# Performance work log

Hardware: AMD Instinct MI355X
Metric: run time of the kernel (lower is better)

The kernel has to match this reference:

```python
import jax, jax.numpy as jnp
import numpy as np

V, C, L, H, FF, T_MAX = 50257, 768, 12, 12, 3072, 1024
D = C // H  # head_dim = 64
B, T = 4, 1024


def setup_inputs() -> dict:
    key = jax.random.key(0)
    ks = jax.random.split(key, 20)
    s = 0.02
    inp = {
        'input_ids': jax.random.randint(ks[0], (B, T), 0, V),
        'tok_emb': jax.random.normal(ks[1], (V, C), jnp.float32) * s,
        'pos_emb': jax.random.normal(ks[2], (T_MAX, C), jnp.float32) * s,
        # per-layer stacked params; linear weights stored [in, out] (torch W.T)
        'qkv_w': jax.random.normal(ks[3], (L, C, 3 * C), jnp.float32) * s,
        'qkv_b': jnp.zeros((L, 3 * C), jnp.float32),
        'proj_w': jax.random.normal(ks[4], (L, C, C), jnp.float32) * (s / np.sqrt(2 * L)),
        'proj_b': jnp.zeros((L, C), jnp.float32),
        'ln1_w': jnp.ones((L, C), jnp.float32),
        'ln1_b': jnp.zeros((L, C), jnp.float32),
        'ln2_w': jnp.ones((L, C), jnp.float32),
        'ln2_b': jnp.zeros((L, C), jnp.float32),
        'fc1_w': jax.random.normal(ks[5], (L, C, FF), jnp.float32) * s,
        'fc1_b': jnp.zeros((L, FF), jnp.float32),
        'fc2_w': jax.random.normal(ks[6], (L, FF, C), jnp.float32) * s,
        'fc2_b': jnp.zeros((L, C), jnp.float32),
        'lnf_w': jnp.ones((C,), jnp.float32),
        'lnf_b': jnp.zeros((C,), jnp.float32),
    }
    return inp


def _ln(x, w, b, eps=1e-5):
    mu = jnp.mean(x, axis=-1, keepdims=True)
    var = jnp.var(x, axis=-1, keepdims=True)
    return (x - mu) * jax.lax.rsqrt(var + eps) * w + b


def _gpt_forward(input_ids, tok_emb, pos_emb, qkv_w, qkv_b, proj_w, proj_b,
                 ln1_w, ln1_b, ln2_w, ln2_b, fc1_w, fc1_b, fc2_w, fc2_b,
                 lnf_w, lnf_b):
    Bc, Tc = input_ids.shape
    x = tok_emb[input_ids] + pos_emb[:Tc][None, :, :]  # [B,T,C]
    causal = jnp.tril(jnp.ones((Tc, Tc), bool))  # [T,T]
    scale = 1.0 / np.sqrt(D)

    def block(x, p):
        (qw, qb, pw, pb, l1w, l1b, l2w, l2b, f1w, f1b, f2w, f2b) = p
        h = _ln(x, l1w, l1b)
        qkv = h @ qw + qb  # [B,T,3C]
        q, k, v = jnp.split(qkv, 3, axis=-1)
        q = q.reshape(Bc, Tc, H, D)
        k = k.reshape(Bc, Tc, H, D)
        v = v.reshape(Bc, Tc, H, D)
        att = jnp.einsum('bqhd,bkhd->bhqk', q, k) * scale
        att = jnp.where(causal[None, None], att, -jnp.inf)
        att = jax.nn.softmax(att, axis=-1)
        o = jnp.einsum('bhqk,bkhd->bqhd', att, v).reshape(Bc, Tc, C)
        x = x + o @ pw + pb
        h2 = _ln(x, l2w, l2b)
        m = jax.nn.gelu(h2 @ f1w + f1b, approximate=False) @ f2w + f2b
        return x + m, None

    params = (qkv_w, qkv_b, proj_w, proj_b, ln1_w, ln1_b, ln2_w, ln2_b,
              fc1_w, fc1_b, fc2_w, fc2_b)
    x, _ = jax.lax.scan(block, x, params)
    x = _ln(x, lnf_w, lnf_b)
    logits = x @ tok_emb.T  # tied lm_head, no bias
    return logits


def reference(input_ids, tok_emb, pos_emb, qkv_w, qkv_b, proj_w, proj_b,
              ln1_w, ln1_b, ln2_w, ln2_b, fc1_w, fc1_b, fc2_w, fc2_b,
              lnf_w, lnf_b):
    return _gpt_forward(input_ids, tok_emb, pos_emb, qkv_w, qkv_b, proj_w,
                        proj_b, ln1_w, ln1_b, ln2_w, ln2_b, fc1_w, fc1_b,
                        fc2_w, fc2_b, lnf_w, lnf_b)
```

## Files before the change

### kernel.cpp

```cpp
#include <hip/hip_runtime.h>
#include <hip/hip_bf16.h>


typedef __bf16 bh_t;
typedef __bf16 bfx4 __attribute__((ext_vector_type(4)));
typedef __bf16 bfx8 __attribute__((ext_vector_type(8)));
typedef float  fx4  __attribute__((ext_vector_type(4)));

#define CDIM 768
#define TSEQ 1024
#define NHEAD 12
#define HDIM 64
#define NLAYER 12
#define MROWS 4096
#define VOCAB 50257
#define VPAD  50432

__device__ __forceinline__ void gload_lds16(const void* g, void* l) {
  __builtin_amdgcn_global_load_lds(
      (const __attribute__((address_space(1))) void*)g,
      (__attribute__((address_space(3))) void*)l, 16, 0, 0);
}

__device__ __forceinline__ fx4 mfma16(bfx8 a, bfx8 b, fx4 c) {
  return __builtin_amdgcn_mfma_f32_16x16x32_bf16(a, b, c, 0, 0, 0);
}

__global__ __launch_bounds__(512, 1) void gemm256(
    const bh_t* __restrict__ A, const bh_t* __restrict__ B,
    const float* __restrict__ bias, void* __restrict__ outp,
    int M, int N, int K, int lda, int flags)
{
  __shared__ bh_t LA0[2][128][64], LB0[2][128][64];
  __shared__ bh_t LA1[2][128][64], LB1[2][128][64];
  const int tid = threadIdx.x;
  const int wid = tid >> 6, lane = tid & 63;
  const int g = lane >> 4, r16 = lane & 15;
  const int wr = wid >> 2, wc = wid & 3;
  const int m0 = blockIdx.x * 256, n0 = blockIdx.y * 256;
  const int sw0 = ((g     ) ^ (r16 & 7)) * 8;
  const int sw1 = ((g + 4) ^ (r16 & 7)) * 8;

  const bh_t* Ab = A + (size_t)blockIdx.z * K + (size_t)m0 * lda;
  const bh_t* Bb = B + (size_t)blockIdx.z * K + (size_t)n0 * lda;
  const bh_t* Ab1 = Ab + (size_t)128 * lda;
  const bh_t* Bb1 = Bb + (size_t)128 * lda;
  const int nt = K >> 6;

  fx4 acc[8][4] = {};

  auto stageHalf = [&](bh_t* dst, const bh_t* src, int t) {
    const int k0 = t << 6;
    #pragma unroll
    for (int j = 0; j < 2; ++j) {
      const int idx = j * 512 + tid;
      const int row = idx >> 3;
      const int slot = (idx & 7) ^ (row & 7);
      gload_lds16(src + (size_t)row * lda + k0 + slot * 8, dst + (size_t)idx * 8);
    }
  };

#define LM_TILE(CA, CB, NA, NB, T)                                            \
  {                                                                           \
    const bh_t* ca = &CA[wr][0][0];                                           \
    const bh_t* cb = &CB[wc >> 1][0][0] + (size_t)((wc & 1) * 64) * 64;       \
    bfx8 a0[4], b0[4], b1[4];                                                 \
                                       \
    _Pragma("unroll")                                                         \
    for (int ni = 0; ni < 4; ++ni)                                            \
      b0[ni] = *(const bfx8*)(cb + (size_t)(ni * 16 + r16) * 64 + sw0);       \
    _Pragma("unroll")                                                         \
    for (int mi = 0; mi < 4; ++mi)                                            \
      a0[mi] = *(const bfx8*)(ca + (size_t)(mi * 16 + r16) * 64 + sw0);       \
    __builtin_amdgcn_s_setprio(1);                                            \
    _Pragma("unroll")                                                         \
    for (int mi = 0; mi < 4; ++mi)                                            \
      _Pragma("unroll")                                                       \
      for (int ni = 0; ni < 4; ++ni)                                          \
        acc[mi][ni] = mfma16(a0[mi], b0[ni], acc[mi][ni]);                    \
    __builtin_amdgcn_s_setprio(0);                                            \
                                        \
    if ((T) + 1 < nt) stageHalf(&NA[1][0][0], Ab1, (T) + 1);                  \
    _Pragma("unroll")                                                         \
    for (int mi = 0; mi < 4; ++mi)                                            \
      a0[mi] = *(const bfx8*)(ca + (size_t)(64 + mi * 16 + r16) * 64 + sw0);  \
    __builtin_amdgcn_s_setprio(1);                                            \
    _Pragma("unroll")                                                         \
    for (int mi = 0; mi < 4; ++mi)                                            \
      _Pragma("unroll")                                                       \
      for (int ni = 0; ni < 4; ++ni)                                          \
        acc[4 + mi][ni] = mfma16(a0[mi], b0[ni], acc[4 + mi][ni]);            \
    __builtin_amdgcn_s_setprio(0);                                            \
                                \
    if ((T) + 1 < nt) stageHalf(&NB[0][0][0], Bb, (T) + 1);                   \
    _Pragma("unroll")                                                         \
    for (int ni = 0; ni < 4; ++ni)                                            \
      b1[ni] = *(const bfx8*)(cb + (size_t)(ni * 16 + r16) * 64 + sw1);       \
    _Pragma("unroll")                                                         \
    for (int mi = 0; mi < 4; ++mi)                                            \
      a0[mi] = *(const bfx8*)(ca + (size_t)(mi * 16 + r16) * 64 + sw1);       \
    __builtin_amdgcn_s_setprio(1);                                            \
    _Pragma("unroll")                                                         \
    for (int mi = 0; mi < 4; ++mi)                                            \
      _Pragma("unroll")                                                       \
      for (int ni = 0; ni < 4; ++ni)                                          \
        acc[mi][ni] = mfma16(a0[mi], b1[ni], acc[mi][ni]);                    \
    __builtin_amdgcn_s_setprio(0);                                            \
                                        \
    if ((T) + 1 < nt) stageHalf(&NB[1][0][0], Bb1, (T) + 1);                  \
    _Pragma("unroll")                                                         \
    for (int mi = 0; mi < 4; ++mi)                                            \
      a0[mi] = *(const bfx8*)(ca + (size_t)(64 + mi * 16 + r16) * 64 + sw1);  \
    __builtin_amdgcn_s_setprio(1);                                            \
    _Pragma("unroll")                                                         \
    for (int mi = 0; mi < 4; ++mi)                                            \
      _Pragma("unroll")                                                       \
      for (int ni = 0; ni < 4; ++ni)                                          \
        acc[4 + mi][ni] = mfma16(a0[mi], b1[ni], acc[4 + mi][ni]);            \
    __builtin_amdgcn_s_setprio(0);                                            \
                                                                \
    asm volatile("s_waitcnt lgkmcnt(0)" ::: "memory");                        \
    __builtin_amdgcn_s_barrier();                                             \
    if ((T) + 2 < nt) {                                                       \
      stageHalf(&CA[0][0][0], Ab, (T) + 2);                                   \
      asm volatile("s_waitcnt vmcnt(2)" ::: "memory");                        \
    } else if ((T) + 1 < nt) {                                                \
      asm volatile("s_waitcnt vmcnt(0)" ::: "memory");                        \
    }                                                                         \
    __builtin_amdgcn_s_barrier();                                             \
    asm volatile("" ::: "memory");                                            \
  }

  stageHalf(&LA0[0][0][0], Ab, 0);
  stageHalf(&LA0[1][0][0], Ab1, 0);
  stageHalf(&LB0[0][0][0], Bb, 0);
  stageHalf(&LB0[1][0][0], Bb1, 0);
  stageHalf(&LA1[0][0][0], Ab, 1);
  asm volatile("s_waitcnt vmcnt(2)" ::: "memory");
  __builtin_amdgcn_s_barrier();
  asm volatile("" ::: "memory");

  for (int t = 0; t < nt; t += 2) {
    LM_TILE(LA0, LB0, LA1, LB1, t);
    LM_TILE(LA1, LB1, LA0, LB0, t + 1);
  }
#undef LM_TILE

  const bool hasBias = flags & 1, doGelu = flags & 4, outBf = flags & 8;
  float* outF = (float*)outp + (size_t)blockIdx.z * ((size_t)M * N);
  bh_t*  outB = (bh_t*)outp;
  #pragma unroll
  for (int mi = 0; mi < 8; ++mi) {
    const int rowb = m0 + wr * 128 + mi * 16 + 4 * g;
    #pragma unroll
    for (int ni = 0; ni < 4; ++ni) {
      const int col = n0 + wc * 64 + ni * 16 + r16;
      if (col >= N) continue;
      const float bv = hasBias ? bias[col] : 0.0f;
      #pragma unroll
      for (int rr = 0; rr < 4; ++rr) {
        const size_t idx = (size_t)(rowb + rr) * N + col;
        float v = acc[mi][ni][rr] + bv;
        if (doGelu) v = 0.5f * v * (1.0f + erff(v * 0.70710678118654752f));
        if (outBf) outB[idx] = (bh_t)v; else outF[idx] = v;
      }
    }
  }
}

__global__ __launch_bounds__(256, 3) void gemm_bt(
    const bh_t* __restrict__ A, const bh_t* __restrict__ B,
    const float* __restrict__ bias, const float* __restrict__ resid,
    void* __restrict__ outp, int M, int N, int K, int lda, int flags)
{
  __shared__ bh_t As0[4][128][8], Bs0[4][128][8];
  __shared__ bh_t As1[4][128][8], Bs1[4][128][8];
  __shared__ bh_t As2[4][128][8], Bs2[4][128][8];
  const int tid  = threadIdx.x;
  const int wave = tid >> 6, lane = tid & 63;
  const int g = lane >> 4, r16 = lane & 15;
  const int m0 = blockIdx.x * 128, n0 = blockIdx.y * 128;
  const int wm = (wave >> 1) * 64, wn = (wave & 1) * 64;

  const bh_t* Ab = A;
  const bh_t* Bb = B;
  if (gridDim.z > 1) {
    Ab += (size_t)blockIdx.z * K;
    Bb += (size_t)blockIdx.z * K;
  }
  Ab += (size_t)m0 * lda;
  Bb += (size_t)n0 * lda;

  const int row0 = tid & 127, kb0 = tid >> 7;
  const int kb1 = kb0 + 2;

  fx4 acc[4][4] = {};
  const int nk = K >> 5;

  auto stageTo = [&](bh_t* AsF, bh_t* BsF, int t) {
    const int k0 = t << 5;
    gload_lds16(Ab + (size_t)row0 * lda + k0 + kb0 * 8, AsF + (size_t)(wave * 64) * 8);
    gload_lds16(Ab + (size_t)row0 * lda + k0 + kb1 * 8, AsF + (size_t)(256 + wave * 64) * 8);
    gload_lds16(Bb + (size_t)row0 * lda + k0 + kb0 * 8, BsF + (size_t)(wave * 64) * 8);
    gload_lds16(Bb + (size_t)row0 * lda + k0 + kb1 * 8, BsF + (size_t)(256 + wave * 64) * 8);
  };

#define GPT_PHASE(CURA, CURB, NXA, NXB, T)                                   \
  {                                                                          \
    if ((T) + 1 < nk) { asm volatile("s_waitcnt vmcnt(4)" ::: "memory"); }   \
    else              { asm volatile("s_waitcnt vmcnt(0)" ::: "memory"); }   \
    __builtin_amdgcn_s_barrier();                                            \
    asm volatile("" ::: "memory");                                           \
    if ((T) + 2 < nk) stageTo(&NXA[0][0][0], &NXB[0][0][0], (T) + 2);        \
    bfx8 af[4], bfr[4];                                                      \
    _Pragma("unroll")                                                        \
    for (int mi = 0; mi < 4; ++mi)                                           \
      af[mi] = *(const bfx8*)&CURA[g][wm + mi * 16 + r16][0];                \
    _Pragma("unroll")                                                        \
    for (int ni = 0; ni < 4; ++ni)                                           \
      bfr[ni] = *(const bfx8*)&CURB[g][wn + ni * 16 + r16][0];               \
    _Pragma("unroll")                                                        \
    for (int mi = 0; mi < 4; ++mi)                                           \
      _Pragma("unroll")                                                      \
      for (int ni = 0; ni < 4; ++ni)                                         \
        acc[mi][ni] = mfma16(af[mi], bfr[ni], acc[mi][ni]);                  \
  }

  stageTo(&As0[0][0][0], &Bs0[0][0][0], 0);
  stageTo(&As1[0][0][0], &Bs1[0][0][0], 1);
  for (int t = 0; t < nk; t += 3) {
    GPT_PHASE(As0, Bs0, As2, Bs2, t);
    GPT_PHASE(As1, Bs1, As0, Bs0, t + 1);
    GPT_PHASE(As2, Bs2, As1, Bs1, t + 2);
  }
#undef GPT_PHASE

  const bool hasBias = flags & 1, hasRes = flags & 2;
  const bool doGelu  = flags & 4, outBf  = flags & 8;
  float* outF = (float*)outp + (size_t)blockIdx.z * ((size_t)M * N);
  bh_t*  outB = (bh_t*)outp;
  #pragma unroll
  for (int mi = 0; mi < 4; ++mi) {
    #pragma unroll
    for (int ni = 0; ni < 4; ++ni) {
      const int col = n0 + wn + ni * 16 + r16;
      if (col >= N) continue;
      const int rowb = m0 + wm + mi * 16 + 4 * g;
      const float bv = hasBias ? bias[col] : 0.0f;
      #pragma unroll
      for (int rr = 0; rr < 4; ++rr) {
        const size_t idx = (size_t)(rowb + rr) * N + col;
        float v = acc[mi][ni][rr] + bv;
        if (doGelu) v = 0.5f * v * (1.0f + erff(v * 0.70710678118654752f));
        if (hasRes) v += resid[idx];
        if (outBf) outB[idx] = (bh_t)v; else outF[idx] = v;
      }
    }
  }
}

__global__ __launch_bounds__(256) void skred_ln(
    const float* __restrict__ part, const float* __restrict__ bias,
    float* __restrict__ x, const float* __restrict__ w,
    const float* __restrict__ bb, bh_t* __restrict__ out, int S)
{
  const int wave = threadIdx.x >> 6, lane = threadIdx.x & 63;
  const int row = blockIdx.x * 4 + wave;
  const size_t base = (size_t)row * CDIM;
  const int off = lane * 4;
  const size_t stride = (size_t)MROWS * CDIM;

  float4 v0 = *(const float4*)(x + base + off);
  float4 v1 = *(const float4*)(x + base + 256 + off);
  float4 v2 = *(const float4*)(x + base + 512 + off);
  for (int s = 0; s < S; ++s) {
    const float* pr = part + s * stride + base;
    const float4 p0 = *(const float4*)(pr + off);
    const float4 p1 = *(const float4*)(pr + 256 + off);
    const float4 p2 = *(const float4*)(pr + 512 + off);
    v0.x += p0.x; v0.y += p0.y; v0.z += p0.z; v0.w += p0.w;
    v1.x += p1.x; v1.y += p1.y; v1.z += p1.z; v1.w += p1.w;
    v2.x += p2.x; v2.y += p2.y; v2.z += p2.z; v2.w += p2.w;
  }
  const float4 q0 = *(const float4*)(bias + off);
  const float4 q1 = *(const float4*)(bias + 256 + off);
  const float4 q2 = *(const float4*)(bias + 512 + off);
  v0.x += q0.x; v0.y += q0.y; v0.z += q0.z; v0.w += q0.w;
  v1.x += q1.x; v1.y += q1.y; v1.z += q1.z; v1.w += q1.w;
  v2.x += q2.x; v2.y += q2.y; v2.z += q2.z; v2.w += q2.w;
  *(float4*)(x + base + off) = v0;
  *(float4*)(x + base + 256 + off) = v1;
  *(float4*)(x + base + 512 + off) = v2;

  float s1 = v0.x + v0.y + v0.z + v0.w + v1.x + v1.y + v1.z + v1.w
           + v2.x + v2.y + v2.z + v2.w;
  float ss = v0.x*v0.x + v0.y*v0.y + v0.z*v0.z + v0.w*v0.w
           + v1.x*v1.x + v1.y*v1.y + v1.z*v1.z + v1.w*v1.w
           + v2.x*v2.x + v2.y*v2.y + v2.z*v2.z + v2.w*v2.w;
  #pragma unroll
  for (int d = 1; d < 64; d <<= 1) { s1 += __shfl_xor(s1, d); ss += __shfl_xor(ss, d); }
  const float mean = s1 * (1.0f / 768.0f);
  const float inv = rsqrtf(ss * (1.0f / 768.0f) - mean * mean + 1e-5f);
  bh_t* orow = out + base;

  const float4 w0 = *(const float4*)(w + off),       b0 = *(const float4*)(bb + off);
  const float4 w1 = *(const float4*)(w + 256 + off), b1 = *(const float4*)(bb + 256 + off);
  const float4 w2 = *(const float4*)(w + 512 + off), b2 = *(const float4*)(bb + 512 + off);
  bfx4 o;
  o[0] = (bh_t)((v0.x - mean) * inv * w0.x + b0.x);
  o[1] = (bh_t)((v0.y - mean) * inv * w0.y + b0.y);
  o[2] = (bh_t)((v0.z - mean) * inv * w0.z + b0.z);
  o[3] = (bh_t)((v0.w - mean) * inv * w0.w + b0.w);
  *(bfx4*)(orow + off) = o;
  o[0] = (bh_t)((v1.x - mean) * inv * w1.x + b1.x);
  o[1] = (bh_t)((v1.y - mean) * inv * w1.y + b1.y);
  o[2] = (bh_t)((v1.z - mean) * inv * w1.z + b1.z);
  o[3] = (bh_t)((v1.w - mean) * inv * w1.w + b1.w);
  *(bfx4*)(orow + 256 + off) = o;
  o[0] = (bh_t)((v2.x - mean) * inv * w2.x + b2.x);
  o[1] = (bh_t)((v2.y - mean) * inv * w2.y + b2.y);
  o[2] = (bh_t)((v2.z - mean) * inv * w2.z + b2.z);
  o[3] = (bh_t)((v2.w - mean) * inv * w2.w + b2.w);
  *(bfx4*)(orow + 512 + off) = o;
}

__global__ __launch_bounds__(256) void attn_fwd(
    const bh_t* __restrict__ qkv, const bh_t* __restrict__ vT,
    bh_t* __restrict__ outb)
{
  __shared__ bh_t P[4][16][56];
  const int wave = threadIdx.x >> 6, lane = threadIdx.x & 63;
  const int g = lane >> 4, r16 = lane & 15;
  const int gw = blockIdx.x * 4 + wave;
  const int qblk = gw & 63;
  const int bh = gw >> 6;
  const int h = bh % NHEAD, b = bh / NHEAD;
  const int qbase = qblk * 16;
  const int qidx = qbase + r16;

  const bh_t* qp = qkv + (size_t)(b * TSEQ + qbase + r16) * (3 * CDIM) + h * HDIM + 8 * g;
  const bfx8 qf0 = *(const bfx8*)qp;
  const bfx8 qf1 = *(const bfx8*)(qp + 32);

  fx4 o[4] = {};
  float m = -INFINITY, l = 0.0f;
  const int ntiles = qblk / 2 + 1;

  for (int t = 0; t < ntiles; ++t) {
    const int kv0 = t * 32;
    const bh_t* kp = qkv + (size_t)(b * TSEQ + kv0 + r16) * (3 * CDIM) + CDIM + h * HDIM + 8 * g;
    const bfx8 ka0 = *(const bfx8*)kp;
    const bfx8 ka1 = *(const bfx8*)(kp + 32);
    const bfx8 kb0 = *(const bfx8*)(kp + 16 * (3 * CDIM));
    const bfx8 kb1 = *(const bfx8*)(kp + 16 * (3 * CDIM) + 32);
    fx4 s0 = {}, s1 = {};
    s0 = mfma16(ka0, qf0, s0); s0 = mfma16(ka1, qf1, s0);
    s1 = mfma16(kb0, qf0, s1); s1 = mfma16(kb1, qf1, s1);

    float mx = -INFINITY;
    float sv0[4], sv1[4];
    #pragma unroll
    for (int rr = 0; rr < 4; ++rr) {
      const int kva = kv0 + 4 * g + rr;
      const int kvb = kva + 16;
      sv0[rr] = (kva <= qidx) ? s0[rr] * 0.125f : -INFINITY;
      sv1[rr] = (kvb <= qidx) ? s1[rr] * 0.125f : -INFINITY;
      mx = fmaxf(mx, fmaxf(sv0[rr], sv1[rr]));
    }
    mx = fmaxf(mx, __shfl_xor(mx, 16));
    mx = fmaxf(mx, __shfl_xor(mx, 32));
    const float mnew = fmaxf(m, mx);
    const float corr = __expf(m - mnew);

    float ps = 0.0f;
    float pv0[4], pv1[4];
    #pragma unroll
    for (int rr = 0; rr < 4; ++rr) {
      pv0[rr] = __expf(sv0[rr] - mnew);
      pv1[rr] = __expf(sv1[rr] - mnew);
      ps += pv0[rr] + pv1[rr];
    }
    ps += __shfl_xor(ps, 16);
    ps += __shfl_xor(ps, 32);
    l = l * corr + ps;
    m = mnew;

    #pragma unroll
    for (int rr = 0; rr < 4; ++rr) {
      const float cr = __shfl(corr, 4 * g + rr);
      o[0][rr] *= cr; o[1][rr] *= cr; o[2][rr] *= cr; o[3][rr] *= cr;
    }

    bfx4 w0, w1;
    #pragma unroll
    for (int rr = 0; rr < 4; ++rr) { w0[rr] = (bh_t)pv0[rr]; w1[rr] = (bh_t)pv1[rr]; }
    *(bfx4*)&P[wave][r16][4 * g]      = w0;
    *(bfx4*)&P[wave][r16][16 + 4 * g] = w1;
    __builtin_amdgcn_wave_barrier();
    const bfx8 pf = *(const bfx8*)&P[wave][r16][8 * g];

    #pragma unroll
    for (int fi = 0; fi < 4; ++fi) {
      const bh_t* vp = vT + (size_t)(bh * HDIM + fi * 16 + r16) * TSEQ + kv0 + 8 * g;
      const bfx8 vf = *(const bfx8*)vp;
      o[fi] = mfma16(pf, vf, o[fi]);
    }
  }

  #pragma unroll
  for (int rr = 0; rr < 4; ++rr) {
    const float lr = __shfl(l, 4 * g + rr);
    const float inv = 1.0f / lr;
    const int trow = b * TSEQ + qbase + 4 * g + rr;
    #pragma unroll
    for (int fi = 0; fi < 4; ++fi)
      outb[(size_t)trow * CDIM + h * HDIM + fi * 16 + r16] = (bh_t)(o[fi][rr] * inv);
  }
}

__global__ __launch_bounds__(256) void ln_fwd(
    const float* __restrict__ x, const float* __restrict__ w,
    const float* __restrict__ bb, bh_t* __restrict__ out)
{
  const int wave = threadIdx.x >> 6, lane = threadIdx.x & 63;
  const int row = blockIdx.x * 4 + wave;
  const float* xr = x + (size_t)row * CDIM;
  const int off = lane * 4;
  const float4 v0 = *(const float4*)(xr + off);
  const float4 v1 = *(const float4*)(xr + 256 + off);
  const float4 v2 = *(const float4*)(xr + 512 + off);
  float s  = v0.x + v0.y + v0.z + v0.w + v1.x + v1.y + v1.z + v1.w
           + v2.x + v2.y + v2.z + v2.w;
  float ss = v0.x*v0.x + v0.y*v0.y + v0.z*v0.z + v0.w*v0.w
           + v1.x*v1.x + v1.y*v1.y + v1.z*v1.z + v1.w*v1.w
           + v2.x*v2.x + v2.y*v2.y + v2.z*v2.z + v2.w*v2.w;
  #pragma unroll
  for (int d = 1; d < 64; d <<= 1) { s += __shfl_xor(s, d); ss += __shfl_xor(ss, d); }
  const float mean = s * (1.0f / 768.0f);
  const float inv = rsqrtf(ss * (1.0f / 768.0f) - mean * mean + 1e-5f);
  bh_t* orow = out + (size_t)row * CDIM;

  const float4 w0 = *(const float4*)(w + off),  b0 = *(const float4*)(bb + off);
  const float4 w1 = *(const float4*)(w + 256 + off), b1 = *(const float4*)(bb + 256 + off);
  const float4 w2 = *(const float4*)(w + 512 + off), b2 = *(const float4*)(bb + 512 + off);
  bfx4 o;
  o[0] = (bh_t)((v0.x - mean) * inv * w0.x + b0.x);
  o[1] = (bh_t)((v0.y - mean) * inv * w0.y + b0.y);
  o[2] = (bh_t)((v0.z - mean) * inv * w0.z + b0.z);
  o[3] = (bh_t)((v0.w - mean) * inv * w0.w + b0.w);
  *(bfx4*)(orow + off) = o;
  o[0] = (bh_t)((v1.x - mean) * inv * w1.x + b1.x);
  o[1] = (bh_t)((v1.y - mean) * inv * w1.y + b1.y);
  o[2] = (bh_t)((v1.z - mean) * inv * w1.z + b1.z);
  o[3] = (bh_t)((v1.w - mean) * inv * w1.w + b1.w);
  *(bfx4*)(orow + 256 + off) = o;
  o[0] = (bh_t)((v2.x - mean) * inv * w2.x + b2.x);
  o[1] = (bh_t)((v2.y - mean) * inv * w2.y + b2.y);
  o[2] = (bh_t)((v2.z - mean) * inv * w2.z + b2.z);
  o[3] = (bh_t)((v2.w - mean) * inv * w2.w + b2.w);
  *(bfx4*)(orow + 512 + off) = o;
}

__global__ void embed_k(const int* __restrict__ ids, const float* __restrict__ tok,
                        const float* __restrict__ pos, float* __restrict__ x)
{
  const int bt = blockIdx.x;
  const int t = bt & (TSEQ - 1);
  const int id = ids[bt];
  const float* tr = tok + (size_t)id * CDIM;
  const float* pr = pos + (size_t)t * CDIM;
  float* xr = x + (size_t)bt * CDIM;
  for (int j = threadIdx.x; j < CDIM; j += 256) xr[j] = tr[j] + pr[j];
}

__global__ void tconv(const float* __restrict__ in, bh_t* __restrict__ out, int R, int Cn)
{
  __shared__ float tile[32][33];
  const size_t msz = (size_t)R * Cn;
  in  += msz * blockIdx.z;
  out += msz * blockIdx.z;
  const int tx = threadIdx.x & 31, ty = threadIdx.x >> 5;
  const int c0 = blockIdx.x * 32, r0 = blockIdx.y * 32;
  #pragma unroll
  for (int i = 0; i < 32; i += 8)
    tile[ty + i][tx] = in[(size_t)(r0 + ty + i) * Cn + c0 + tx];
  __syncthreads();
  #pragma unroll
  for (int i = 0; i < 32; i += 8)
    out[(size_t)(c0 + ty + i) * R + r0 + tx] = (bh_t)tile[tx][ty + i];
}

__global__ void embconv(const float* __restrict__ in, bh_t* __restrict__ out)
{
  const size_t i4 = ((size_t)blockIdx.x * 256 + threadIdx.x) * 4;
  if (i4 >= (size_t)VPAD * CDIM) return;
  const size_t vlim = (size_t)VOCAB * CDIM;
  float4 f = make_float4(0.f, 0.f, 0.f, 0.f);
  if (i4 < vlim) f = *(const float4*)(in + i4);
  bfx4 o;
  o[0] = (bh_t)f.x; o[1] = (bh_t)f.y; o[2] = (bh_t)f.z; o[3] = (bh_t)f.w;
  *(bfx4*)(out + i4) = o;
}

__global__ void vtrans(const bh_t* __restrict__ qkv, bh_t* __restrict__ vT)
{
  __shared__ bh_t tile[32][34];
  const int bh = blockIdx.z;
  const int b = bh / NHEAD, h = bh % NHEAD;
  const int d0 = blockIdx.x * 32, t0 = blockIdx.y * 32;
  const int tx = threadIdx.x & 31, ty = threadIdx.x >> 5;
  #pragma unroll
  for (int i = 0; i < 32; i += 8)
    tile[ty + i][tx] = qkv[(size_t)(b * TSEQ + t0 + ty + i) * (3 * CDIM) + 2 * CDIM + h * HDIM + d0 + tx];
  __syncthreads();
  #pragma unroll
  for (int i = 0; i < 32; i += 8)
    vT[(size_t)(bh * HDIM + d0 + ty + i) * TSEQ + t0 + tx] = tile[tx][ty + i];
}

extern "C" void kernel_launch(void* const* d_in, const int* in_sizes, int n_in,
                              void* d_out, int out_size, void* d_ws, size_t ws_size,
                              hipStream_t stream)
{
  (void)in_sizes; (void)n_in; (void)out_size; (void)ws_size;
  const int*   ids    = (const int*)d_in[0];
  const float* tok    = (const float*)d_in[1];
  const float* pos    = (const float*)d_in[2];
  const float* qkv_w  = (const float*)d_in[3];
  const float* qkv_b  = (const float*)d_in[4];
  const float* proj_w = (const float*)d_in[5];
  const float* proj_b = (const float*)d_in[6];
  const float* ln1_w  = (const float*)d_in[7];
  const float* ln1_b  = (const float*)d_in[8];
  const float* ln2_w  = (const float*)d_in[9];
  const float* ln2_b  = (const float*)d_in[10];
  const float* fc1_w  = (const float*)d_in[11];
  const float* fc1_b  = (const float*)d_in[12];
  const float* fc2_w  = (const float*)d_in[13];
  const float* fc2_b  = (const float*)d_in[14];
  const float* lnf_w  = (const float*)d_in[15];
  const float* lnf_b  = (const float*)d_in[16];

  char* wp = (char*)d_ws;
  auto carve = [&](size_t bytes) { char* p = wp; wp += (bytes + 255) & ~(size_t)255; return p; };
  float* x     = (float*)carve((size_t)MROWS * CDIM * 4);
  bh_t*  hbuf  = (bh_t*)carve((size_t)MROWS * CDIM * 2);
  bh_t*  qkvb  = (bh_t*)carve((size_t)MROWS * 3 * CDIM * 2);
  bh_t*  vT    = (bh_t*)carve((size_t)48 * HDIM * TSEQ * 2);
  bh_t*  attno = (bh_t*)carve((size_t)MROWS * CDIM * 2);
  bh_t*  mlp1  = (bh_t*)carve((size_t)MROWS * 3072 * 2);
  bh_t*  embT  = (bh_t*)carve((size_t)VPAD * CDIM * 2);

  char* op = (char*)d_out;
  auto carveO = [&](size_t bytes) { char* p = op; op += (bytes + 255) & ~(size_t)255; return p; };
  bh_t* qkvwT  = (bh_t*)carveO((size_t)NLAYER * 3 * CDIM * CDIM * 2);
  bh_t* projwT = (bh_t*)carveO((size_t)NLAYER * CDIM * CDIM * 2);
  bh_t* fc1wT  = (bh_t*)carveO((size_t)NLAYER * 3072 * CDIM * 2);
  bh_t* fc2wT  = (bh_t*)carveO((size_t)NLAYER * CDIM * 3072 * 2);
  float* skpart = (float*)carveO((size_t)4 * MROWS * CDIM * 4);

  tconv<<<dim3(2304 / 32, 768 / 32, NLAYER), 256, 0, stream>>>(qkv_w, qkvwT, 768, 2304);
  tconv<<<dim3(768 / 32, 768 / 32, NLAYER), 256, 0, stream>>>(proj_w, projwT, 768, 768);
  tconv<<<dim3(3072 / 32, 768 / 32, NLAYER), 256, 0, stream>>>(fc1_w, fc1wT, 768, 3072);
  tconv<<<dim3(768 / 32, 3072 / 32, NLAYER), 256, 0, stream>>>(fc2_w, fc2wT, 3072, 768);
  embconv<<<((VPAD * CDIM / 4) + 255) / 256, 256, 0, stream>>>(tok, embT);
  embed_k<<<MROWS, 256, 0, stream>>>(ids, tok, pos, x);

  ln_fwd<<<MROWS / 4, 256, 0, stream>>>(x, ln1_w, ln1_b, hbuf);
  for (int l = 0; l < NLAYER; ++l) {
    gemm256<<<dim3(16, 9), 512, 0, stream>>>(hbuf, qkvwT + (size_t)l * 3 * CDIM * CDIM,
        qkv_b + l * 3 * CDIM, qkvb, MROWS, 3 * CDIM, CDIM, CDIM, 1 | 8);
    vtrans<<<dim3(2, 32, 48), 256, 0, stream>>>(qkvb, vT);
    attn_fwd<<<768, 256, 0, stream>>>(qkvb, vT, attno);
    gemm_bt<<<dim3(32, 6, 4), 256, 0, stream>>>(attno,
        projwT + (size_t)l * CDIM * CDIM, nullptr, nullptr,
        skpart, MROWS, CDIM, 192, CDIM, 0);
    skred_ln<<<MROWS / 4, 256, 0, stream>>>(skpart, proj_b + l * CDIM, x,
        ln2_w + l * CDIM, ln2_b + l * CDIM, hbuf, 4);
    gemm256<<<dim3(16, 12), 512, 0, stream>>>(hbuf, fc1wT + (size_t)l * 3072 * CDIM,
        fc1_b + l * 3072, mlp1, MROWS, 3072, CDIM, CDIM, 1 | 4 | 8);
    gemm256<<<dim3(16, 3, 4), 512, 0, stream>>>(mlp1, fc2wT + (size_t)l * CDIM * 3072,
        nullptr, skpart, MROWS, CDIM, 768, 3072, 0);
    const float* nw = (l + 1 < NLAYER) ? ln1_w + (l + 1) * CDIM : lnf_w;
    const float* nb = (l + 1 < NLAYER) ? ln1_b + (l + 1) * CDIM : lnf_b;
    skred_ln<<<MROWS / 4, 256, 0, stream>>>(skpart, fc2_b + l * CDIM, x, nw, nb, hbuf, 4);
  }
  gemm256<<<dim3(16, VPAD / 256), 512, 0, stream>>>(hbuf, embT, nullptr,
      (float*)d_out, MROWS, VOCAB, CDIM, CDIM, 0);
}
```

Measured before the change: 3.942 ms.

## Restructure GEMM pipeline to stage full tiles after compute with per-phase barriers

Result: slower. 4.177 ms (+6.0%).

```diff
diff --git a/kernel.cpp b/kernel.cpp
--- a/kernel.cpp
+++ b/kernel.cpp
@@ -38,11 +38,11 @@
   const int g = lane >> 4, r16 = lane & 15;
   const int wr = wid >> 2, wc = wid & 3;
   const int m0 = blockIdx.x * 256, n0 = blockIdx.y * 256;
-  const int sw0 = ((g     ) ^ (r16 & 7)) * 8;
+  const int sw0 = ((g    ) ^ (r16 & 7)) * 8;
   const int sw1 = ((g + 4) ^ (r16 & 7)) * 8;
 
-  const bh_t* Ab = A + (size_t)blockIdx.z * K + (size_t)m0 * lda;
-  const bh_t* Bb = B + (size_t)blockIdx.z * K + (size_t)n0 * lda;
+  const bh_t* Ab  = A + (size_t)blockIdx.z * K + (size_t)m0 * lda;
+  const bh_t* Bb  = B + (size_t)blockIdx.z * K + (size_t)n0 * lda;
   const bh_t* Ab1 = Ab + (size_t)128 * lda;
   const bh_t* Bb1 = Bb + (size_t)128 * lda;
   const int nt = K >> 6;
@@ -60,91 +60,83 @@
     }
   };
 
-#define LM_TILE(CA, CB, NA, NB, T)                                            \
+#define LM_PHASE_MFMA(AOFS, BREG, ACCOFS)                                     \
+    __builtin_amdgcn_s_barrier();                                             \
+    asm volatile("s_waitcnt lgkmcnt(0)" ::: "memory");                        \
+    __builtin_amdgcn_s_setprio(1);                                            \
+    _Pragma("unroll")                                                         \
+    for (int mi = 0; mi < 4; ++mi)                                            \
+      _Pragma("unroll")                                                       \
+      for (int ni = 0; ni < 4; ++ni)                                          \
+        acc[(ACCOFS) + mi][ni] = mfma16(av[mi], BREG[ni], acc[(ACCOFS) + mi][ni]); \
+    __builtin_amdgcn_s_setprio(0);                                            \
+    __builtin_amdgcn_s_barrier();
+
+#define LM_TILE(CA, CB, T)                                                    \
   {                                                                           \
     const bh_t* ca = &CA[wr][0][0];                                           \
     const bh_t* cb = &CB[wc >> 1][0][0] + (size_t)((wc & 1) * 64) * 64;       \
-    bfx8 a0[4], b0[4], b1[4];                                                 \
-                                       \
+    bfx8 av[4], b0[4], b1[4];                                                 \
+                                \
     _Pragma("unroll")                                                         \
     for (int ni = 0; ni < 4; ++ni)                                            \
       b0[ni] = *(const bfx8*)(cb + (size_t)(ni * 16 + r16) * 64 + sw0);       \
     _Pragma("unroll")                                                         \
     for (int mi = 0; mi < 4; ++mi)                                            \
-      a0[mi] = *(const bfx8*)(ca + (size_t)(mi * 16 + r16) * 64 + sw0);       \
-    __builtin_amdgcn_s_setprio(1);                                            \
+      av[mi] = *(const bfx8*)(ca + (size_t)(mi * 16 + r16) * 64 + sw0);       \
+    LM_PHASE_MFMA(0, b0, 0)                                                   \
+                                      \
     _Pragma("unroll")                                                         \
     for (int mi = 0; mi < 4; ++mi)                                            \
-      _Pragma("unroll")                                                       \
-      for (int ni = 0; ni < 4; ++ni)                                          \
-        acc[mi][ni] = mfma16(a0[mi], b0[ni], acc[mi][ni]);                    \
-    __builtin_amdgcn_s_setprio(0);                                            \
-                                        \
-    if ((T) + 1 < nt) stageHalf(&NA[1][0][0], Ab1, (T) + 1);                  \
-    _Pragma("unroll")                                                         \
-    for (int mi = 0; mi < 4; ++mi)                                            \
-      a0[mi] = *(const bfx8*)(ca + (size_t)(64 + mi * 16 + r16) * 64 + sw0);  \
-    __builtin_amdgcn_s_setprio(1);                                            \
-    _Pragma("unroll")                                                         \
-    for (int mi = 0; mi < 4; ++mi)                                            \
-      _Pragma("unroll")                                                       \
-      for (int ni = 0; ni < 4; ++ni)                                          \
-        acc[4 + mi][ni] = mfma16(a0[mi], b0[ni], acc[4 + mi][ni]);            \
-    __builtin_amdgcn_s_setprio(0);                                            \
+      av[mi] = *(const bfx8*)(ca + (size_t)(64 + mi * 16 + r16) * 64 + sw0);  \
+    LM_PHASE_MFMA(64, b0, 4)                                                  \
                                 \
-    if ((T) + 1 < nt) stageHalf(&NB[0][0][0], Bb, (T) + 1);                   \
     _Pragma("unroll")                                                         \
     for (int ni = 0; ni < 4; ++ni)                                            \
       b1[ni] = *(const bfx8*)(cb + (size_t)(ni * 16 + r16) * 64 + sw1);       \
     _Pragma("unroll")                                                         \
     for (int mi = 0; mi < 4; ++mi)                                            \
-      a0[mi] = *(const bfx8*)(ca + (size_t)(mi * 16 + r16) * 64 + sw1);       \
-    __builtin_amdgcn_s_setprio(1);                                            \
+      av[mi] = *(const bfx8*)(ca + (size_t)(mi * 16 + r16) * 64 + sw1);       \
+    LM_PHASE_MFMA(0, b1, 0)                                                   \
+                                      \
     _Pragma("unroll")                                                         \
     for (int mi = 0; mi < 4; ++mi)                                            \
-      _Pragma("unroll")                                                       \
-      for (int ni = 0; ni < 4; ++ni)                                          \
-        acc[mi][ni] = mfma16(a0[mi], b1[ni], acc[mi][ni]);                    \
-    __builtin_amdgcn_s_setprio(0);                                            \
-                                        \
-    if ((T) + 1 < nt) stageHalf(&NB[1][0][0], Bb1, (T) + 1);                  \
-    _Pragma("unroll")                                                         \
-    for (int mi = 0; mi < 4; ++mi)                                            \
-      a0[mi] = *(const bfx8*)(ca + (size_t)(64 + mi * 16 + r16) * 64 + sw1);  \
-    __builtin_amdgcn_s_setprio(1);                                            \
-    _Pragma("unroll")                                                         \
-    for (int mi = 0; mi < 4; ++mi)                                            \
-      _Pragma("unroll")                                                       \
-      for (int ni = 0; ni < 4; ++ni)                                          \
-        acc[4 + mi][ni] = mfma16(a0[mi], b1[ni], acc[4 + mi][ni]);            \
-    __builtin_amdgcn_s_setprio(0);                                            \
-                                                                \
-    asm volatile("s_waitcnt lgkmcnt(0)" ::: "memory");                        \
-    __builtin_amdgcn_s_barrier();                                             \
+      av[mi] = *(const bfx8*)(ca + (size_t)(64 + mi * 16 + r16) * 64 + sw1);  \
+    LM_PHASE_MFMA(64, b1, 4)                                                  \
+       \
     if ((T) + 2 < nt) {                                                       \
-      stageHalf(&CA[0][0][0], Ab, (T) + 2);                                   \
-      asm volatile("s_waitcnt vmcnt(2)" ::: "memory");                        \
+      stageHalf(&CA[0][0][0], Ab,  (T) + 2);                                  \
+      stageHalf(&CA[1][0][0], Ab1, (T) + 2);                                  \
+      stageHalf(&CB[0][0][0], Bb,  (T) + 2);                                  \
+      stageHalf(&CB[1][0][0], Bb1, (T) + 2);                                  \
+      asm volatile("s_waitcnt vmcnt(8)" ::: "memory");                        \
     } else if ((T) + 1 < nt) {                                                \
       asm volatile("s_waitcnt vmcnt(0)" ::: "memory");                        \
     }                                                                         \
-    __builtin_amdgcn_s_barrier();                                             \
-    asm volatile("" ::: "memory");                                            \
-  }
-
-  stageHalf(&LA0[0][0][0], Ab, 0);
+    if ((T) + 1 < nt) {                                                       \
+      __builtin_amdgcn_s_barrier();                                           \
+      asm volatile("" ::: "memory");                                          \
+    }                                                                         \
+  }
+
+  stageHalf(&LA0[0][0][0], Ab,  0);
   stageHalf(&LA0[1][0][0], Ab1, 0);
-  stageHalf(&LB0[0][0][0], Bb, 0);
+  stageHalf(&LB0[0][0][0], Bb,  0);
   stageHalf(&LB0[1][0][0], Bb1, 0);
-  stageHalf(&LA1[0][0][0], Ab, 1);
-  asm volatile("s_waitcnt vmcnt(2)" ::: "memory");
+  stageHalf(&LA1[0][0][0], Ab,  1);
+  stageHalf(&LA1[1][0][0], Ab1, 1);
+  stageHalf(&LB1[0][0][0], Bb,  1);
+  stageHalf(&LB1[1][0][0], Bb1, 1);
+  asm volatile("s_waitcnt vmcnt(8)" ::: "memory");
   __builtin_amdgcn_s_barrier();
   asm volatile("" ::: "memory");
 
   for (int t = 0; t < nt; t += 2) {
-    LM_TILE(LA0, LB0, LA1, LB1, t);
-    LM_TILE(LA1, LB1, LA0, LB0, t + 1);
+    LM_TILE(LA0, LB0, t);
+    LM_TILE(LA1, LB1, t + 1);
   }
 #undef LM_TILE
+#undef LM_PHASE_MFMA
 
   const bool hasBias = flags & 1, doGelu = flags & 4, outBf = flags & 8;
   float* outF = (float*)outp + (size_t)blockIdx.z * ((size_t)M * N);
```

## Add 256x128-tile GEMM kernel with small LDS footprint for QKV and FC1

Applied to the files above, without the earlier changes.

After: 3.823 ms. 1.03x faster.

```diff
diff --git a/kernel.cpp b/kernel.cpp
--- a/kernel.cpp
+++ b/kernel.cpp
@@ -38,11 +38,11 @@
   const int g = lane >> 4, r16 = lane & 15;
   const int wr = wid >> 2, wc = wid & 3;
   const int m0 = blockIdx.x * 256, n0 = blockIdx.y * 256;
-  const int sw0 = ((g     ) ^ (r16 & 7)) * 8;
+  const int sw0 = ((g    ) ^ (r16 & 7)) * 8;
   const int sw1 = ((g + 4) ^ (r16 & 7)) * 8;
 
-  const bh_t* Ab = A + (size_t)blockIdx.z * K + (size_t)m0 * lda;
-  const bh_t* Bb = B + (size_t)blockIdx.z * K + (size_t)n0 * lda;
+  const bh_t* Ab  = A + (size_t)blockIdx.z * K + (size_t)m0 * lda;
+  const bh_t* Bb  = B + (size_t)blockIdx.z * K + (size_t)n0 * lda;
   const bh_t* Ab1 = Ab + (size_t)128 * lda;
   const bh_t* Bb1 = Bb + (size_t)128 * lda;
   const int nt = K >> 6;
@@ -65,7 +65,6 @@
     const bh_t* ca = &CA[wr][0][0];                                           \
     const bh_t* cb = &CB[wc >> 1][0][0] + (size_t)((wc & 1) * 64) * 64;       \
     bfx8 a0[4], b0[4], b1[4];                                                 \
-                                       \
     _Pragma("unroll")                                                         \
     for (int ni = 0; ni < 4; ++ni)                                            \
       b0[ni] = *(const bfx8*)(cb + (size_t)(ni * 16 + r16) * 64 + sw0);       \
@@ -79,7 +78,6 @@
       for (int ni = 0; ni < 4; ++ni)                                          \
         acc[mi][ni] = mfma16(a0[mi], b0[ni], acc[mi][ni]);                    \
     __builtin_amdgcn_s_setprio(0);                                            \
-                                        \
     if ((T) + 1 < nt) stageHalf(&NA[1][0][0], Ab1, (T) + 1);                  \
     _Pragma("unroll")                                                         \
     for (int mi = 0; mi < 4; ++mi)                                            \
@@ -91,7 +89,6 @@
       for (int ni = 0; ni < 4; ++ni)                                          \
         acc[4 + mi][ni] = mfma16(a0[mi], b0[ni], acc[4 + mi][ni]);            \
     __builtin_amdgcn_s_setprio(0);                                            \
-                                \
     if ((T) + 1 < nt) stageHalf(&NB[0][0][0], Bb, (T) + 1);                   \
     _Pragma("unroll")                                                         \
     for (int ni = 0; ni < 4; ++ni)                                            \
@@ -106,7 +103,6 @@
       for (int ni = 0; ni < 4; ++ni)                                          \
         acc[mi][ni] = mfma16(a0[mi], b1[ni], acc[mi][ni]);                    \
     __builtin_amdgcn_s_setprio(0);                                            \
-                                        \
     if ((T) + 1 < nt) stageHalf(&NB[1][0][0], Bb1, (T) + 1);                  \
     _Pragma("unroll")                                                         \
     for (int mi = 0; mi < 4; ++mi)                                            \
@@ -118,7 +114,6 @@
       for (int ni = 0; ni < 4; ++ni)                                          \
         acc[4 + mi][ni] = mfma16(a0[mi], b1[ni], acc[4 + mi][ni]);            \
     __builtin_amdgcn_s_setprio(0);                                            \
-                                                                \
     asm volatile("s_waitcnt lgkmcnt(0)" ::: "memory");                        \
     __builtin_amdgcn_s_barrier();                                             \
     if ((T) + 2 < nt) {                                                       \
@@ -155,6 +150,99 @@
     #pragma unroll
     for (int ni = 0; ni < 4; ++ni) {
       const int col = n0 + wc * 64 + ni * 16 + r16;
+      if (col >= N) continue;
+      const float bv = hasBias ? bias[col] : 0.0f;
+      #pragma unroll
+      for (int rr = 0; rr < 4; ++rr) {
+        const size_t idx = (size_t)(rowb + rr) * N + col;
+        float v = acc[mi][ni][rr] + bv;
+        if (doGelu) v = 0.5f * v * (1.0f + erff(v * 0.70710678118654752f));
+        if (outBf) outB[idx] = (bh_t)v; else outF[idx] = v;
+      }
+    }
+  }
+}
+
+__global__ __launch_bounds__(512, 4) void gemm256n(
+    const bh_t* __restrict__ A, const bh_t* __restrict__ B,
+    const float* __restrict__ bias, void* __restrict__ outp,
+    int M, int N, int K, int lda, int flags)
+{
+  __shared__ bh_t A0[256][32], B0s[128][32];
+  __shared__ bh_t A1[256][32], B1s[128][32];
+  const int tid = threadIdx.x;
+  const int wid = tid >> 6, lane = tid & 63;
+  const int g = lane >> 4, r16 = lane & 15;
+  const int wr = wid >> 2, wc = wid & 3;
+  const int m0 = blockIdx.x * 256, n0 = blockIdx.y * 128;
+  const int swk = (g ^ ((r16 >> 1) & 3)) * 8;
+
+  const bh_t* Ab = A + (size_t)m0 * lda;
+  const bh_t* Bb = B + (size_t)n0 * lda;
+  const int nt = K >> 5;
+
+  fx4 acc[8][2] = {};
+
+  auto stage = [&](bh_t* dA, bh_t* dB, int t) {
+    const int k0 = t << 5;
+    #pragma unroll
+    for (int j = 0; j < 2; ++j) {
+      const int idx = j * 512 + tid;
+      const int row = idx >> 2;
+      const int slot = (idx & 3) ^ ((row >> 1) & 3);
+      gload_lds16(Ab + (size_t)row * lda + k0 + slot * 8, dA + (size_t)idx * 8);
+    }
+    {
+      const int idx = tid;
+      const int row = idx >> 2;
+      const int slot = (idx & 3) ^ ((row >> 1) & 3);
+      gload_lds16(Bb + (size_t)row * lda + k0 + slot * 8, dB + (size_t)idx * 8);
+    }
+  };
+
+#define N_TILE(CA, CB, NA, NB, T)                                             \
+  {                                                                           \
+    if ((T) + 1 < nt) stage(&NA[0][0], &NB[0][0], (T) + 1);                   \
+    bfx8 av[8], bv[2];                                                        \
+    _Pragma("unroll")                                                         \
+    for (int ni = 0; ni < 2; ++ni)                                            \
+      bv[ni] = *(const bfx8*)(&CB[wc * 32 + ni * 16 + r16][0] + swk);         \
+    _Pragma("unroll")                                                         \
+    for (int mi = 0; mi < 8; ++mi)                                            \
+      av[mi] = *(const bfx8*)(&CA[wr * 128 + mi * 16 + r16][0] + swk);        \
+    asm volatile("s_waitcnt lgkmcnt(0)" ::: "memory");                        \
+    __builtin_amdgcn_s_setprio(1);                                            \
+    _Pragma("unroll")                                                         \
+    for (int mi = 0; mi < 8; ++mi)                                            \
+      _Pragma("unroll")                                                       \
+      for (int ni = 0; ni < 2; ++ni)                                          \
+        acc[mi][ni] = mfma16(av[mi], bv[ni], acc[mi][ni]);                    \
+    __builtin_amdgcn_s_setprio(0);                                            \
+    asm volatile("s_waitcnt vmcnt(0)" ::: "memory");                          \
+    __builtin_amdgcn_s_barrier();                                             \
+    asm volatile("" ::: "memory");                                            \
+  }
+
+  stage(&A0[0][0], &B0s[0][0], 0);
+  asm volatile("s_waitcnt vmcnt(0)" ::: "memory");
+  __builtin_amdgcn_s_barrier();
+  asm volatile("" ::: "memory");
+
+  for (int t = 0; t < nt; t += 2) {
+    N_TILE(A0, B0s, A1, B1s, t);
+    N_TILE(A1, B1s, A0, B0s, t + 1);
+  }
+#undef N_TILE
+
+  const bool hasBias = flags & 1, doGelu = flags & 4, outBf = flags & 8;
+  float* outF = (float*)outp;
+  bh_t*  outB = (bh_t*)outp;
+  #pragma unroll
+  for (int mi = 0; mi < 8; ++mi) {
+    const int rowb = m0 + wr * 128 + mi * 16 + 4 * g;
+    #pragma unroll
+    for (int ni = 0; ni < 2; ++ni) {
+      const int col = n0 + wc * 32 + ni * 16 + r16;
       if (col >= N) continue;
       const float bv = hasBias ? bias[col] : 0.0f;
       #pragma unroll
@@ -568,7 +656,7 @@
 
   ln_fwd<<<MROWS / 4, 256, 0, stream>>>(x, ln1_w, ln1_b, hbuf);
   for (int l = 0; l < NLAYER; ++l) {
-    gemm256<<<dim3(16, 9), 512, 0, stream>>>(hbuf, qkvwT + (size_t)l * 3 * CDIM * CDIM,
+    gemm256n<<<dim3(16, 18), 512, 0, stream>>>(hbuf, qkvwT + (size_t)l * 3 * CDIM * CDIM,
         qkv_b + l * 3 * CDIM, qkvb, MROWS, 3 * CDIM, CDIM, CDIM, 1 | 8);
     vtrans<<<dim3(2, 32, 48), 256, 0, stream>>>(qkvb, vT);
     attn_fwd<<<768, 256, 0, stream>>>(qkvb, vT, attno);
@@ -577,7 +665,7 @@
         skpart, MROWS, CDIM, 192, CDIM, 0);
     skred_ln<<<MROWS / 4, 256, 0, stream>>>(skpart, proj_b + l * CDIM, x,
         ln2_w + l * CDIM, ln2_b + l * CDIM, hbuf, 4);
-    gemm256<<<dim3(16, 12), 512, 0, stream>>>(hbuf, fc1wT + (size_t)l * 3072 * CDIM,
+    gemm256n<<<dim3(16, 24), 512, 0, stream>>>(hbuf, fc1wT + (size_t)l * 3072 * CDIM,
         fc1_b + l * 3072, mlp1, MROWS, 3072, CDIM, CDIM, 1 | 4 | 8);
     gemm256<<<dim3(16, 3, 4), 512, 0, stream>>>(mlp1, fc2wT + (size_t)l * CDIM * 3072,
         nullptr, skpart, MROWS, CDIM, 768, 3072, 0);
```
